# Optimization experiments

Measured on AMD Instinct MI355X. Metric: run time of the kernel, lower is better.

Reference implementation:

```python
import jax, jax.numpy as jnp
import numpy as np
import math

B, S, SIG, EMB, LAT, H, L_ENC, L_DEC = 16, 1024, 256, 256, 256, 8, 2, 2
EH, DH = EMB // H, LAT // H
EPS = 1e-10


def _sinusoidal_last_row(d):
    # last row of a standard sinusoidal PE table (position index = max_len-1)
    pos = 5000.0 - 1.0
    i = np.arange(d)
    angles = pos / np.power(10000.0, (2 * (i // 2)) / d)
    pe = np.where(i % 2 == 0, np.sin(angles), np.cos(angles))
    return jnp.asarray(pe, dtype=jnp.float32)


def setup_inputs() -> dict:
    key = jax.random.key(0)
    ks = iter(jax.random.split(key, 64))
    w = lambda *sh: 0.05 * jax.random.normal(next(ks), sh, dtype=jnp.float32)
    z = lambda *sh: jnp.zeros(sh, dtype=jnp.float32)
    d = {
        'inputData': jax.random.normal(next(ks), (B, S, SIG), dtype=jnp.float32),
        'pos_enc': _sinusoidal_last_row(SIG),
        'embW': w(SIG, EMB), 'embb': z(EMB),
        'qW': w(EMB, EMB), 'qb': z(EMB),
        'kW': w(EMB, EMB), 'kb': z(EMB),
        'vW': w(EMB, EMB), 'vb': z(EMB),
        'encBW': w(EH, EH), 'encBb': z(EH),
        'oW': w(EMB, EMB), 'ob': z(EMB),
        'ffe_W1': w(EMB, 2 * EMB), 'ffe_b1': z(2 * EMB),
        'ffe_W2': w(2 * EMB, EMB), 'ffe_b2': z(EMB),
        'lnSA_g': jnp.ones((L_ENC, EMB)), 'lnSA_b': z(L_ENC, EMB),
        'lnFF_g': jnp.ones((L_ENC, EMB)), 'lnFF_b': z(L_ENC, EMB),
        'start': w(1, LAT),
        'decQW': w(LAT, LAT), 'decQb': z(LAT),
        'decKW': w(EMB, EMB), 'decKb': z(EMB),
        'decVW': w(EMB, LAT), 'decVb': z(LAT),
        'decBW': w(EH + DH, DH), 'decBb': z(DH),
        'latW': w(LAT, LAT), 'latb': z(LAT),
        'ffd_W1': w(LAT, LAT // 2), 'ffd_b1': z(LAT // 2),
        'ffd_W2': w(LAT // 2, LAT), 'ffd_b2': z(LAT),
        'lnCA_g': jnp.ones((L_DEC, LAT)), 'lnCA_b': z(L_DEC, LAT),
        'lnLFF_g': jnp.ones((L_DEC, LAT)), 'lnLFF_b': z(L_DEC, LAT),
        'finW': w(LAT, LAT), 'finb': z(LAT),
    }
    return d


def _ln(x, g, b):
    m = x.mean(-1, keepdims=True)
    v = x.var(-1, keepdims=True)
    return (x - m) * jax.lax.rsqrt(v + EPS) * g + b


def _enc_attn(x, qW, qb, kW, kb, vW, vb, bW, bb, oW, ob):
    # x: (B,S,EMB) -> heads (B,H,S,EH)
    sp = lambda t: t.reshape(B, S, H, EH).transpose(0, 2, 1, 3)
    q, k, v = sp(x @ qW + qb), sp(x @ kW + kb), sp(x @ vW + vb)
    bk = k @ bW + bb                                   # bilinear key (B,H,S,EH)
    attn = jax.nn.softmax(jnp.einsum('bhqd,bhkd->bhqk', q, bk) / math.sqrt(EH), axis=-1)
    out = jnp.einsum('bhqk,bhkd->bhqd', attn, v)
    out = out.transpose(0, 2, 1, 3).reshape(B, S, EMB)
    return out @ oW + ob


def _dec_attn(enc, lat, qW, qb, kW, kb, vW, vb, bW, bb, oW, ob):
    # lat: (B,LAT) single query token; enc: (B,S,EMB)
    q = (lat @ qW + qb).reshape(B, 1, H, DH).transpose(0, 2, 1, 3)   # (B,H,1,DH)
    k = (enc @ kW + kb).reshape(B, S, H, EH).transpose(0, 2, 1, 3)   # (B,H,S,EH)
    v = (enc @ vW + vb).reshape(B, S, H, DH).transpose(0, 2, 1, 3)   # (B,H,S,DH)
    qcat = jnp.broadcast_to(q, (B, H, S, DH))
    kcat = jnp.concatenate([k, qcat], axis=-1)                       # (B,H,S,EH+DH)
    bk = kcat @ bW + bb                                              # (B,H,S,DH)
    attn = jax.nn.softmax(jnp.einsum('bhqd,bhkd->bhqk', q, bk) / math.sqrt(EH + DH), axis=-1)
    out = jnp.einsum('bhqk,bhkd->bhqd', attn, v)                     # (B,H,1,DH)
    out = out.transpose(0, 2, 1, 3).reshape(B, LAT)
    return out @ oW + ob


def reference(inputData, pos_enc, embW, embb, qW, qb, kW, kb, vW, vb, encBW, encBb,
              oW, ob, ffe_W1, ffe_b1, ffe_W2, ffe_b2, lnSA_g, lnSA_b, lnFF_g, lnFF_b,
              start, decQW, decQb, decKW, decKb, decVW, decVb, decBW, decBb,
              latW, latb, ffd_W1, ffd_b1, ffd_W2, ffd_b2, lnCA_g, lnCA_b,
              lnLFF_g, lnLFF_b, finW, finb):
    emb = (inputData + pos_enc) @ embW + embb          # (B,S,EMB)
    t = emb
    for l in range(L_ENC):
        n = _ln(t, lnSA_g[l], lnSA_b[l])
        a = _enc_attn(n, qW, qb, kW, kb, vW, vb, encBW, encBb, oW, ob) + n
        t = a + emb
        n2 = _ln(t, lnFF_g[l], lnFF_b[l])
        ff = jax.nn.selu(n2 @ ffe_W1 + ffe_b1) @ ffe_W2 + ffe_b2
        t = ff + n2
    init_lat = jnp.broadcast_to(start, (B, LAT))
    lat = init_lat
    for l in range(L_DEC):
        nl = _ln(init_lat, lnCA_g[l], lnCA_b[l])       # module always feeds initialLatentData
        lat = _dec_attn(t, nl, decQW, decQb, decKW, decKb, decVW, decVb,
                        decBW, decBb, latW, latb)
        nf = _ln(lat, lnLFF_g[l], lnLFF_b[l])
        lat = jax.nn.selu(nf @ ffd_W1 + ffd_b1) @ ffd_W2 + ffd_b2
    return lat @ finW + finb
```

## Files before the change

kernel.cpp:

```cpp
#include <hip/hip_runtime.h>
#include <hip/hip_bf16.h>
#include <math.h>

typedef __hip_bfloat16 bf16;

#define BB 16
#define SS 1024
#define NH 8
#define NR (BB*SS)
#define SZE ((size_t)NR*256)
#define RS 264
#define HS 520
#define KS2 136

typedef __attribute__((ext_vector_type(8))) short short8;
typedef __attribute__((ext_vector_type(4))) float f32x4;
typedef __attribute__((ext_vector_type(8))) unsigned short u16x8;
typedef __attribute__((ext_vector_type(4))) unsigned short u16x4;

__device__ __forceinline__ float bf2f(bf16 x){ return __bfloat162float(x); }
__device__ __forceinline__ bf16  f2bf(float x){ return __float2bfloat16(x); }
__device__ __forceinline__ unsigned short f2bfu(float x){
  bf16 t = __float2bfloat16(x); return *reinterpret_cast<unsigned short*>(&t);
}
__device__ __forceinline__ float bfu2f(unsigned short u){
  return __uint_as_float(((unsigned)u)<<16);
}

__device__ __forceinline__ float ldT(const float* p, size_t i){ return p[i]; }
__device__ __forceinline__ float ldT(const bf16*  p, size_t i){ return bf2f(p[i]); }
__device__ __forceinline__ void  stT(float* p, size_t i, float v){ p[i] = v; }
__device__ __forceinline__ void  stT(bf16*  p, size_t i, float v){ p[i] = f2bf(v); }

__device__ __forceinline__ float selu_f(float x){
  const float a = 1.6732632423543772f, sc = 1.0507009873554805f;
  return sc * (x > 0.f ? x : a * expm1f(x));
}

__device__ __forceinline__ void gload16(const void* g, void* l){
  __builtin_amdgcn_global_load_lds(
      (const __attribute__((address_space(1))) unsigned int*)g,
      (__attribute__((address_space(3))) unsigned int*)l, 16, 0, 0);
}

struct PtrPack { const void* p[43]; };
struct TabPack { int off[43]; int cnt[43]; int total; };
struct TrTab   { int srcOff[12]; int K[12]; int N[12]; int dstOff[12]; int total; };

__global__ __launch_bounds__(256) void k_canon(PtrPack ptrs, TabPack tab,
    float* __restrict__ dst, int* __restrict__ flagw)
{
  unsigned w0 = ((const unsigned*)ptrs.p[18])[0];
  int isbf = (w0 == 0x3F803F80u) ? 1 : 0;
  if (blockIdx.x == 0 && threadIdx.x == 0) *flagw = isbf;
  __shared__ int so[43], sn[43];
  int tid = threadIdx.x;
  if (tid < 43){ so[tid] = tab.off[tid]; sn[tid] = tab.cnt[tid]; }
  __syncthreads();
  int g = blockIdx.x*256 + tid;
  if (g >= tab.total) return;
  int seg = 1;
  while (seg < 42 && g >= so[seg] + sn[seg]) seg++;
  int li = g - so[seg];
  float v = isbf ? bf2f(((const bf16*)ptrs.p[seg])[li])
                 : ((const float*)ptrs.p[seg])[li];
  dst[g] = v;
}

__global__ __launch_bounds__(256) void k_transW(const float* __restrict__ wt,
    TrTab tt, unsigned short* __restrict__ dst)
{
  int g = blockIdx.x*256 + threadIdx.x;
  if (g >= tt.total) return;
  int seg = 0;
  while (seg < 11 && g >= tt.dstOff[seg] + tt.K[seg]*tt.N[seg]) seg++;
  int li = g - tt.dstOff[seg];
  int K = tt.K[seg], N = tt.N[seg];
  int n = li / K, k = li - n*K;
  dst[g] = f2bfu(wt[tt.srcOff[seg] + (size_t)k*N + n]);
}

template<int K, int LDA, int CT>
__device__ __forceinline__ void wave_gemmN(const unsigned short (*As)[LDA],
    const unsigned short* __restrict__ Wt, int n0, f32x4 acc[4][CT], int lane)
{
  int col = lane & 15, quad = lane >> 4;
  #pragma unroll
  for (int k0 = 0; k0 < K; k0 += 32){
    short8 a[4], b[CT];
    #pragma unroll
    for (int rt = 0; rt < 4; rt++)
      a[rt] = *(const short8*)(&As[rt*16 + col][k0 + quad*8]);
    #pragma unroll
    for (int ct = 0; ct < CT; ct++)
      b[ct] = *(const short8*)(&Wt[(size_t)(n0 + ct*16 + col)*K + k0 + quad*8]);
    #pragma unroll
    for (int rt = 0; rt < 4; rt++)
      #pragma unroll
      for (int ct = 0; ct < CT; ct++)
        acc[rt][ct] = __builtin_amdgcn_mfma_f32_16x16x32_bf16(a[rt], b[ct], acc[rt][ct], 0, 0, 0);
  }
}

template<int K, int LDA, int CT>
__device__ __forceinline__ void wave_gemmM32(const unsigned short (*As)[LDA],
    const unsigned short* __restrict__ Wt, int n0, f32x4 acc[2][CT], int lane)
{
  int col = lane & 15, quad = lane >> 4;
  #pragma unroll
  for (int k0 = 0; k0 < K; k0 += 32){
    short8 a[2], b[CT];
    #pragma unroll
    for (int rt = 0; rt < 2; rt++)
      a[rt] = *(const short8*)(&As[rt*16 + col][k0 + quad*8]);
    #pragma unroll
    for (int ct = 0; ct < CT; ct++)
      b[ct] = *(const short8*)(&Wt[(size_t)(n0 + ct*16 + col)*K + k0 + quad*8]);
    #pragma unroll
    for (int rt = 0; rt < 2; rt++)
      #pragma unroll
      for (int ct = 0; ct < CT; ct++)
        acc[rt][ct] = __builtin_amdgcn_mfma_f32_16x16x32_bf16(a[rt], b[ct], acc[rt][ct], 0, 0, 0);
  }
}

#define ZERO_ACC4(acc)  { _Pragma("unroll") for (int rt=0;rt<4;rt++){ _Pragma("unroll") for (int ct=0;ct<4;ct++) acc[rt][ct] = (f32x4){0.f,0.f,0.f,0.f}; } }
#define ZERO_ACC2(acc)  { _Pragma("unroll") for (int rt=0;rt<4;rt++){ _Pragma("unroll") for (int ct=0;ct<2;ct++) acc[rt][ct] = (f32x4){0.f,0.f,0.f,0.f}; } }
#define ZERO_ACC24(acc) { _Pragma("unroll") for (int rt=0;rt<2;rt++){ _Pragma("unroll") for (int ct=0;ct<4;ct++) acc[rt][ct] = (f32x4){0.f,0.f,0.f,0.f}; } }

#define EPI_BEGIN(e) { int rt = (e)>>4, ct = ((e)>>2)&3, r = (e)&3; \
    int lrow = rt*16 + quad*4 + r; int gcol0 = ct*16 + col; \
    float av = acc[rt][ct][r]; (void)lrow; (void)gcol0; (void)av;
#define EPI_END }

#define EPI32_BEGIN(e) { int rt = (e)>>4, ct = ((e)>>2)&3, r = (e)&3; \
    int lrow = rt*16 + quad*4 + r; int gcol0 = ct*16 + col; \
    float av = acc[rt][ct][r]; (void)lrow; (void)gcol0; (void)av;
#define EPI32_END }

template<int PRE, typename OT>
__global__ __launch_bounds__(256) void k_gemm_mfma(const void* __restrict__ A,
    const int* __restrict__ flagp, const float* __restrict__ pe,
    const unsigned short* __restrict__ Wt, const float* __restrict__ bias,
    OT* __restrict__ out)
{
  __shared__ __align__(16) unsigned short As[64][RS];
  int tid = threadIdx.x;
  int m = blockIdx.x & 255, nh = blockIdx.x >> 8;
  int row0 = m*64;
  if (PRE == 0){
    int f = *flagp;
    for (int jj = 0; jj < 64; jj++){
      int idx = tid + jj*256, row = idx>>8, c = idx&255;
      size_t g = (size_t)(row0+row)*256 + c;
      float x = f ? bf2f(((const bf16*)A)[g]) : ((const float*)A)[g];
      As[row][c] = f2bfu(x + pe[c]);
    }
  } else {
    for (int jj = 0; jj < 64; jj++){
      int idx = tid + jj*256, row = idx>>8, c = idx&255;
      As[row][c] = f2bfu(((const float*)A)[(size_t)(row0+row)*256 + c]);
    }
  }
  __syncthreads();
  int w = tid>>6, lane = tid&63, col = lane&15, quad = lane>>4;
  int n0 = nh*128 + w*32;
  f32x4 acc[4][2];
  ZERO_ACC2(acc);
  wave_gemmN<256, RS, 2>(As, Wt, n0, acc, lane);
  #pragma unroll
  for (int rt = 0; rt < 4; rt++){
    #pragma unroll
    for (int ct = 0; ct < 2; ct++){
      #pragma unroll
      for (int r = 0; r < 4; r++){
        int grow = row0 + rt*16 + quad*4 + r;
        int gcol = n0 + ct*16 + col;
        stT(out, (size_t)grow*256 + gcol, acc[rt][ct][r] + bias[gcol]);
      }
    }
  }
}

__global__ __launch_bounds__(256) void k_decKV(const float* __restrict__ A,
    const unsigned short* __restrict__ KWt, const float* __restrict__ kb,
    const unsigned short* __restrict__ VWt, const float* __restrict__ vb,
    bf16* __restrict__ ko, bf16* __restrict__ vo)
{
  __shared__ __align__(16) unsigned short As[64][RS];
  int tid = threadIdx.x;
  int m = blockIdx.x & 255, nh = blockIdx.x >> 8;
  int row0 = m*64;
  for (int jj = 0; jj < 64; jj++){
    int idx = tid + jj*256, row = idx>>8, c = idx&255;
    As[row][c] = f2bfu(A[(size_t)(row0+row)*256 + c]);
  }
  __syncthreads();
  int w = tid>>6, lane = tid&63, col = lane&15, quad = lane>>4;
  int n0 = nh*128 + w*32;
  f32x4 acc[4][2];
  ZERO_ACC2(acc);
  wave_gemmN<256, RS, 2>(As, KWt, n0, acc, lane);
  #pragma unroll
  for (int rt = 0; rt < 4; rt++){
    #pragma unroll
    for (int ct = 0; ct < 2; ct++){
      #pragma unroll
      for (int r = 0; r < 4; r++){
        int grow = row0 + rt*16 + quad*4 + r;
        int gcol = n0 + ct*16 + col;
        ko[(size_t)grow*256 + gcol] = f2bf(acc[rt][ct][r] + kb[gcol]);
      }
    }
  }
  ZERO_ACC2(acc);
  wave_gemmN<256, RS, 2>(As, VWt, n0, acc, lane);
  #pragma unroll
  for (int rt = 0; rt < 4; rt++){
    #pragma unroll
    for (int ct = 0; ct < 2; ct++){
      #pragma unroll
      for (int r = 0; r < 4; r++){
        int grow = row0 + rt*16 + quad*4 + r;
        int gcol = n0 + ct*16 + col;
        vo[(size_t)grow*256 + gcol] = f2bf(acc[rt][ct][r] + vb[gcol]);
      }
    }
  }
}

__global__ __launch_bounds__(256) void k_qkvbk_mfma(const float* __restrict__ tsrc,
    const float* __restrict__ lng, const float* __restrict__ lnb,
    const unsigned short* __restrict__ qWt, const float* __restrict__ qb,
    const unsigned short* __restrict__ kWt, const float* __restrict__ kb,
    const unsigned short* __restrict__ vWt, const float* __restrict__ vb,
    const unsigned short* __restrict__ encBWt, const float* __restrict__ Bb,
    bf16* __restrict__ qo, bf16* __restrict__ vo, bf16* __restrict__ bko)
{
  __shared__ __align__(16) unsigned short Ns[64][RS];
  __shared__ __align__(16) unsigned short Ks[64][KS2];
  __shared__ float mArr[64], rArr[64];
  int tid = threadIdx.x;
  int m = blockIdx.x & 255, nh = blockIdx.x >> 8;
  int row0 = m*64;
  int b = row0 >> 10, s0 = row0 & 1023;
  {
    int row = tid>>2, l4 = tid&3;
    const float* rp = tsrc + (size_t)(row0+row)*256;
    float s = 0.f, s2 = 0.f;
    for (int c = l4; c < 256; c += 4){ float x = rp[c]; s += x; s2 += x*x; }
    s  += __shfl_down(s, 2, 4);  s  += __shfl_down(s, 1, 4);
    s2 += __shfl_down(s2, 2, 4); s2 += __shfl_down(s2, 1, 4);
    if (l4 == 0){
      float mn = s*(1.f/256.f);
      float v = s2*(1.f/256.f) - mn*mn;
      mArr[row] = mn; rArr[row] = rsqrtf(fmaxf(v,0.f) + 1e-10f);
    }
  }
  __syncthreads();
  for (int jj = 0; jj < 64; jj++){
    int idx = tid + jj*256, row = idx>>8, c = idx&255;
    float x = tsrc[(size_t)(row0+row)*256 + c];
    Ns[row][c] = f2bfu((x - mArr[row])*rArr[row]*lng[c] + lnb[c]);
  }
  __syncthreads();
  int w = tid>>6, lane = tid&63, col = lane&15, quad = lane>>4;
  int n0 = nh*128 + w*32;
  f32x4 acc[4][2];
  ZERO_ACC2(acc);
  wave_gemmN<256, RS, 2>(Ns, qWt, n0, acc, lane);
  #pragma unroll
  for (int rt = 0; rt < 4; rt++){
    #pragma unroll
    for (int ct = 0; ct < 2; ct++){
      #pragma unroll
      for (int r = 0; r < 4; r++){
        int grow = row0 + rt*16 + quad*4 + r;
        int gcol = n0 + ct*16 + col;
        qo[(size_t)grow*256 + gcol] = f2bf(acc[rt][ct][r] + qb[gcol]);
      }
    }
  }
  ZERO_ACC2(acc);
  wave_gemmN<256, RS, 2>(Ns, vWt, n0, acc, lane);
  #pragma unroll
  for (int rt = 0; rt < 4; rt++){
    #pragma unroll
    for (int ct = 0; ct < 2; ct++){
      #pragma unroll
      for (int r = 0; r < 4; r++){
        int grow = row0 + rt*16 + quad*4 + r;
        int gcol = n0 + ct*16 + col;
        vo[(size_t)grow*256 + gcol] = f2bf(acc[rt][ct][r] + vb[gcol]);
      }
    }
  }
  ZERO_ACC2(acc);
  wave_gemmN<256, RS, 2>(Ns, kWt, n0, acc, lane);
  #pragma unroll
  for (int rt = 0; rt < 4; rt++){
    #pragma unroll
    for (int ct = 0; ct < 2; ct++){
      #pragma unroll
      for (int r = 0; r < 4; r++){
        int lrow = rt*16 + quad*4 + r;
        int lcol = w*32 + ct*16 + col;
        Ks[lrow][lcol] = f2bfu(acc[rt][ct][r] + kb[nh*128 + lcol]);
      }
    }
  }
  __syncthreads();
  int h = nh*4 + w;
  ZERO_ACC2(acc);
  #pragma unroll
  for (int ct = 0; ct < 2; ct++){
    short8 bfrag = *(const short8*)(&encBWt[(size_t)(ct*16 + col)*32 + quad*8]);
    #pragma unroll
    for (int rt = 0; rt < 4; rt++){
      short8 afrag = *(const short8*)(&Ks[rt*16 + col][w*32 + quad*8]);
      acc[rt][ct] = __builtin_amdgcn_mfma_f32_16x16x32_bf16(afrag, bfrag, acc[rt][ct], 0, 0, 0);
    }
  }
  #pragma unroll
  for (int rt = 0; rt < 4; rt++){
    #pragma unroll
    for (int ct = 0; ct < 2; ct++){
      #pragma unroll
      for (int r = 0; r < 4; r++){
        int srow = s0 + rt*16 + quad*4 + r;
        int d = ct*16 + col;
        bko[(((size_t)(b*NH+h))*SS + srow)*32 + d] = f2bf(acc[rt][ct][r] + Bb[d]);
      }
    }
  }
}

__global__ __launch_bounds__(256) void k_attn_mfma(
    const bf16* __restrict__ q, const bf16* __restrict__ bk,
    const bf16* __restrict__ v, bf16* __restrict__ ao)
{
  int bi = blockIdx.x;
  int qq = bi >> 7, b = (bi >> 3) & 15, h = bi & 7;
  int tid = threadIdx.x;
  int w = tid>>6, lane = tid&63;
  int quad = lane>>4, col = lane&15;
  int q0 = qq*256 + w*64;

  __shared__ __align__(16) unsigned short Ks2b[2][64][32];
  __shared__ __align__(16) unsigned short Vt2b[2][32][72];
  __shared__ __align__(16) unsigned short Ps[4][64][72];

  const float scale2 = 0.17677669529663687f * 1.4426950408889634f;
  short8 aq[4];
  #pragma unroll
  for (int rt = 0; rt < 4; rt++){
    const unsigned short* gq = (const unsigned short*)q
        + ((size_t)(b*SS + q0 + rt*16 + col))*256 + h*32 + quad*8;
    u16x8 qv = *(const u16x8*)gq;
    #pragma unroll
    for (int i=0;i<8;i++) aq[rt][i] = (short)f2bfu(bfu2f(qv[i])*scale2);
  }

  float l_r[4][4];
  f32x4 o0[4], o1[4];
  #pragma unroll
  for (int rt=0;rt<4;rt++){
    o0[rt] = (f32x4){0.f,0.f,0.f,0.f};
    o1[rt] = (f32x4){0.f,0.f,0.f,0.f};
    #pragma unroll
    for (int r=0;r<4;r++) l_r[rt][r] = 0.f;
  }

  u16x8 rK;
  u16x4 rV0, rV1;
  int vk0 = (tid>>3), vdg = (tid&7);
  int vk1 = ((tid+256)>>3), vdg1 = (tid&7);
  {
    const u16x8* srcK = (const u16x8*)((const unsigned short*)bk
        + (((size_t)(b*NH+h))*SS + 0)*32);
    rK = srcK[tid];
    rV0 = *(const u16x4*)((const unsigned short*)v
        + ((size_t)(b*SS + 0 + vk0))*256 + h*32 + vdg*4);
    rV1 = *(const u16x4*)((const unsigned short*)v
        + ((size_t)(b*SS + 0 + vk1))*256 + h*32 + vdg1*4);
  }

  for (int kt = 0; kt < 16; kt++){
    int cb = kt & 1;
    ((u16x8*)&Ks2b[cb][0][0])[tid] = rK;
    #pragma unroll
    for (int i=0;i<4;i++) Vt2b[cb][vdg*4+i][vk0] = rV0[i];
    #pragma unroll
    for (int i=0;i<4;i++) Vt2b[cb][vdg1*4+i][vk1] = rV1[i];
    __syncthreads();
    if (kt < 15){
      int nk = kt + 1;
      const u16x8* srcK = (const u16x8*)((const unsigned short*)bk
          + (((size_t)(b*NH+h))*SS + (size_t)nk*64)*32);
      rK = srcK[tid];
      rV0 = *(const u16x4*)((const unsigned short*)v
          + ((size_t)(b*SS + nk*64 + vk0))*256 + h*32 + vdg*4);
      rV1 = *(const u16x4*)((const unsigned short*)v
          + ((size_t)(b*SS + nk*64 + vk1))*256 + h*32 + vdg1*4);
    }
    short8 bk8[4];
    #pragma unroll
    for (int t4 = 0; t4 < 4; t4++)
      bk8[t4] = *(const short8*)(&Ks2b[cb][t4*16 + col][quad*8]);
    #pragma unroll
    for (int rt = 0; rt < 4; rt++){
      f32x4 s[4];
      #pragma unroll
      for (int t4 = 0; t4 < 4; t4++)
        s[t4] = __builtin_amdgcn_mfma_f32_16x16x32_bf16(aq[rt], bk8[t4],
                  (f32x4){0.f,0.f,0.f,0.f}, 0, 0, 0);
      #pragma unroll
      for (int r=0;r<4;r++){
        #pragma unroll
        for (int t4=0;t4<4;t4++){
          float pv = __builtin_amdgcn_exp2f(s[t4][r]);
          l_r[rt][r] += pv;
          Ps[w][rt*16 + quad*4 + r][t4*16 + col] =
              (unsigned short)(__float_as_uint(pv) >> 16);
        }
      }
    }
    short8 bv00 = *(const short8*)(&Vt2b[cb][col][quad*8]);
    short8 bv10 = *(const short8*)(&Vt2b[cb][col][32 + quad*8]);
    short8 bv01 = *(const short8*)(&Vt2b[cb][16+col][quad*8]);
    short8 bv11 = *(const short8*)(&Vt2b[cb][16+col][32 + quad*8]);
    #pragma unroll
    for (int rt = 0; rt < 4; rt++){
      short8 ap0 = *(const short8*)(&Ps[w][rt*16 + col][quad*8]);
      short8 ap1 = *(const short8*)(&Ps[w][rt*16 + col][32 + quad*8]);
      o0[rt] = __builtin_amdgcn_mfma_f32_16x16x32_bf16(ap0, bv00, o0[rt], 0, 0, 0);
      o0[rt] = __builtin_amdgcn_mfma_f32_16x16x32_bf16(ap1, bv10, o0[rt], 0, 0, 0);
      o1[rt] = __builtin_amdgcn_mfma_f32_16x16x32_bf16(ap0, bv01, o1[rt], 0, 0, 0);
      o1[rt] = __builtin_amdgcn_mfma_f32_16x16x32_bf16(ap1, bv11, o1[rt], 0, 0, 0);
    }
  }
  #pragma unroll
  for (int rt=0;rt<4;rt++){
    #pragma unroll
    for (int r=0;r<4;r++){
      float l = l_r[rt][r];
      #pragma unroll
      for (int msk=1; msk<16; msk<<=1) l += __shfl_xor(l, msk, 64);
      float inv = 1.f / l;
      int qrow = q0 + rt*16 + quad*4 + r;
      size_t o = ((size_t)(b*SS + qrow))*256 + h*32;
      ao[o + col]      = f2bf(o0[rt][r]*inv);
      ao[o + 16 + col] = f2bf(o1[rt][r]*inv);
    }
  }
}

__global__ __launch_bounds__(256) void k_oln_mfma(
    const float* __restrict__ tsrc, const float* __restrict__ emb,
    const bf16* __restrict__ ao,
    const float* __restrict__ lnSAg, const float* __restrict__ lnSAb,
    const unsigned short* __restrict__ oWt, const float* __restrict__ ob,
    const float* __restrict__ lnFFg, const float* __restrict__ lnFFb,
    bf16* __restrict__ n2o)
{
  __shared__ __align__(16) unsigned short Aos[32][RS];
  __shared__ __align__(16) unsigned short Tm[32][RS];
  __shared__ float mArr[32], rArr[32];
  int tid = threadIdx.x, row0 = blockIdx.x*32;
  {
    int row = tid>>3, l8 = tid&7;
    const float* rp = tsrc + (size_t)(row0+row)*256;
    float s = 0.f, s2 = 0.f;
    for (int c = l8; c < 256; c += 8){ float x = rp[c]; s += x; s2 += x*x; }
    s  += __shfl_down(s, 4, 8);  s  += __shfl_down(s, 2, 8);  s  += __shfl_down(s, 1, 8);
    s2 += __shfl_down(s2, 4, 8); s2 += __shfl_down(s2, 2, 8); s2 += __shfl_down(s2, 1, 8);
    if (l8 == 0){
      float m = s*(1.f/256.f);
      float v = s2*(1.f/256.f) - m*m;
      mArr[row] = m; rArr[row] = rsqrtf(fmaxf(v,0.f) + 1e-10f);
    }
  }
  for (int jj = 0; jj < 4; jj++){
    int idx = tid + jj*256;
    int row = idx>>5, c8 = idx&31;
    *(u16x8*)(&Aos[row][c8*8]) =
        *(const u16x8*)((const unsigned short*)ao + (size_t)(row0+row)*256 + c8*8);
  }
  __syncthreads();
  int w = tid>>6, lane = tid&63, col = lane&15, quad = lane>>4;
  f32x4 acc[2][4];
  ZERO_ACC24(acc);
  wave_gemmM32<256, RS, 4>(Aos, oWt, w*64, acc, lane);
  #pragma unroll
  for (int e = 0; e < 32; e++){
    EPI32_BEGIN(e)
    int gcol = w*64 + gcol0;
    size_t g = (size_t)(row0+lrow)*256 + gcol;
    float n1 = (tsrc[g] - mArr[lrow])*rArr[lrow]*lnSAg[gcol] + lnSAb[gcol];
    Tm[lrow][gcol] = f2bfu(av + ob[gcol] + n1 + emb[g]);
    EPI32_END
  }
  __syncthreads();
  {
    int row = tid>>3, l8 = tid&7;
    float s = 0.f, s2 = 0.f;
    for (int c = l8; c < 256; c += 8){ float x = bfu2f(Tm[row][c]); s += x; s2 += x*x; }
    s  += __shfl_down(s, 4, 8);  s  += __shfl_down(s, 2, 8);  s  += __shfl_down(s, 1, 8);
    s2 += __shfl_down(s2, 4, 8); s2 += __shfl_down(s2, 2, 8); s2 += __shfl_down(s2, 1, 8);
    if (l8 == 0){
      float m = s*(1.f/256.f);
      float v = s2*(1.f/256.f) - m*m;
      mArr[row] = m; rArr[row] = rsqrtf(fmaxf(v,0.f) + 1e-10f);
    }
  }
  __syncthreads();
  for (int jj = 0; jj < 32; jj++){
    int idx = tid + jj*256, row = idx>>8, c = idx&255;
    float x = bfu2f(Tm[row][c]);
    n2o[(size_t)(row0+row)*256 + c] =
        f2bf((x - mArr[row])*rArr[row]*lnFFg[c] + lnFFb[c]);
  }
}

#define FF_STAGE(B, KT) { \
  int k0 = (KT)*64; \
  _Pragma("unroll") \
  for (int i = 0; i < 4; i++){ int c = w*4 + i; \
    gload16(A  + (size_t)(row0 + c*8 + rsub)*KFULL + k0 + sgo, &As[B][c*512]); } \
  _Pragma("unroll") \
  for (int i = 0; i < 2; i++){ int c = w*2 + i; \
    gload16(Wb + (size_t)(n0   + c*8 + rsub)*KFULL + k0 + sgo, &Bs[B][c*512]); } }

#define FF_COMPUTE(B) { \
  _Pragma("unroll") \
  for (int kk = 0; kk < 2; kk++){ \
    short8 a[4], b2r[2]; \
    _Pragma("unroll") \
    for (int rt = 0; rt < 4; rt++) \
      a[rt] = *(const short8*)(&As[B][((wr*64 + rt*16 + col)<<6) + ((((kk<<2)|quad) ^ (col&7))<<3)]); \
    _Pragma("unroll") \
    for (int ct = 0; ct < 2; ct++) \
      b2r[ct] = *(const short8*)(&Bs[B][((wc*32 + ct*16 + col)<<6) + ((((kk<<2)|quad) ^ (col&7))<<3)]); \
    _Pragma("unroll") \
    for (int rt = 0; rt < 4; rt++) \
      _Pragma("unroll") \
      for (int ct = 0; ct < 2; ct++) \
        acc[rt][ct] = __builtin_amdgcn_mfma_f32_16x16x32_bf16(a[rt], b2r[ct], acc[rt][ct], 0, 0, 0); } }

template<int KFULL, int NFULL, int EPI>
__global__ __launch_bounds__(256) void k_ff_gemm(const bf16* __restrict__ A,
    const unsigned short* __restrict__ Wt, const float* __restrict__ bias,
    const bf16* __restrict__ res, void* __restrict__ outv)
{
  __shared__ __align__(16) unsigned short As[2][128*64];
  __shared__ __align__(16) unsigned short Bs[2][64*64];
  constexpr int NWG = 128 * (NFULL/64);
  constexpr int NKT = KFULL/64;
  int tid = threadIdx.x;
  int w = tid>>6, lane = tid&63;
  int col = lane&15, quad = lane>>4;
  int wr = w>>1, wc = w&1;
  int rsub = lane>>3;
  int sgo = (((lane&7) ^ rsub)<<3);
  int bid = blockIdx.x;
  int swz = (bid & 7)*(NWG>>3) + (bid >> 3);
  int mb = swz & 127, nb = swz >> 7;
  int row0 = mb*128, n0 = nb*64;
  const bf16* Wb = (const bf16*)Wt;

  f32x4 acc[4][2];
  ZERO_ACC2(acc);

  FF_STAGE(0, 0);
  __syncthreads();
  #pragma unroll
  for (int kt = 0; kt < NKT-1; kt++){
    int cb = kt & 1;
    FF_STAGE(cb^1, kt+1);
    FF_COMPUTE(cb);
    __syncthreads();
  }
  FF_COMPUTE((NKT-1)&1);

  if (EPI == 0){
    bf16* o = (bf16*)outv;
    #pragma unroll
    for (int rt = 0; rt < 4; rt++){
      #pragma unroll
      for (int ct = 0; ct < 2; ct++){
        #pragma unroll
        for (int r = 0; r < 4; r++){
          int grow = row0 + wr*64 + rt*16 + quad*4 + r;
          int gcol = n0 + wc*32 + ct*16 + col;
          o[(size_t)grow*NFULL + gcol] = f2bf(selu_f(acc[rt][ct][r] + bias[gcol]));
        }
      }
    }
  } else {
    float* o = (float*)outv;
    #pragma unroll
    for (int rt = 0; rt < 4; rt++){
      #pragma unroll
      for (int ct = 0; ct < 2; ct++){
        #pragma unroll
        for (int r = 0; r < 4; r++){
          int grow = row0 + wr*64 + rt*16 + quad*4 + r;
          int gcol = n0 + wc*32 + ct*16 + col;
          size_t g = (size_t)grow*NFULL + gcol;
          o[g] = acc[rt][ct][r] + bias[gcol] + bf2f(res[g]);
        }
      }
    }
  }
}

__global__ __launch_bounds__(256) void k_dec_head(const float* __restrict__ startp,
    const float* __restrict__ lng, const float* __restrict__ lnb,
    const float* __restrict__ decQW, const float* __restrict__ decQb,
    const float* __restrict__ decBW,
    float* __restrict__ s_q, float* __restrict__ s_qc)
{
  __shared__ float s1[256], s2[256], nl[256], qv[256];
  int t = threadIdx.x;
  float v = startp[t];
  s1[t]=v; s2[t]=v*v; __syncthreads();
  for (int s=128;s>0;s>>=1){
    if (t<s){ s1[t]+=s1[t+s]; s2[t]+=s2[t+s]; }
    __syncthreads();
  }
  float m = s1[0]*(1.f/256.f);
  float var = s2[0]*(1.f/256.f) - m*m;
  float r = rsqrtf(fmaxf(var,0.f) + 1e-10f);
  nl[t] = (v-m)*r*lng[t] + lnb[t];
  __syncthreads();
  float acc = decQb[t];
  for (int k=0;k<256;k++) acc += nl[k]*decQW[k*256+t];
  qv[t] = acc; s_q[t] = acc;
  __syncthreads();
  int h = t>>5, d = t&31;
  float a = 0.f;
  #pragma unroll 8
  for (int e=0;e<32;e++) a += qv[h*32+e]*decBW[(32+e)*32 + d];
  s_qc[t] = a;
}

__global__ __launch_bounds__(256) void k_bkdec_mfma(const bf16* __restrict__ kk,
    const float* __restrict__ qc, const unsigned short* __restrict__ decBWt,
    const float* __restrict__ Bb, bf16* __restrict__ bko)
{
  __shared__ __align__(16) unsigned short Ks[64][RS];
  int tid = threadIdx.x, row0 = blockIdx.x*64;
  int b = row0 >> 10, s0 = row0 & 1023;
  for (int jj = 0; jj < 8; jj++){
    int idx = tid + jj*256;
    int row = idx>>5, c8 = idx&31;
    *(u16x8*)(&Ks[row][c8*8]) =
        *(const u16x8*)((const unsigned short*)kk + (size_t)(row0+row)*256 + c8*8);
  }
  __syncthreads();
  int w = tid>>6, lane = tid&63, col = lane&15, quad = lane>>4;
  f32x4 acc[4][4];
  ZERO_ACC4(acc);
  #pragma unroll
  for (int ct = 0; ct < 4; ct++){
    int base = w*64 + ct*16;
    int h = base >> 5, d0 = base & 31;
    short8 bfrag = *(const short8*)(&decBWt[(size_t)(d0 + col)*32 + quad*8]);
    #pragma unroll
    for (int rt = 0; rt < 4; rt++){
      short8 afrag = *(const short8*)(&Ks[rt*16 + col][h*32 + quad*8]);
      acc[rt][ct] = __builtin_amdgcn_mfma_f32_16x16x32_bf16(afrag, bfrag, acc[rt][ct], 0, 0, 0);
    }
  }
  #pragma unroll
  for (int e = 0; e < 64; e++){
    EPI_BEGIN(e)
    int srow = s0 + lrow;
    int gcol = w*64 + gcol0;
    int h = gcol >> 5, d = gcol & 31;
    bko[(((size_t)(b*NH+h))*SS + srow)*32 + d] = f2bf(av + qc[gcol] + Bb[d]);
    EPI_END
  }
}

__global__ __launch_bounds__(256) void k_attn_dec(const float* __restrict__ q,
    const bf16* __restrict__ bk, const bf16* __restrict__ v,
    float* __restrict__ out)
{
  int h = blockIdx.x & 7, b = blockIdx.x >> 3;
  int tid = threadIdx.x;
  __shared__ float qs[32];
  __shared__ float sc[SS];
  __shared__ float red[256];
  if (tid < 32) qs[tid] = q[h*32 + tid] * (0.125f * 1.4426950408889634f);
  __syncthreads();
  float lsum = 0.f;
  for (int jj=0;jj<4;jj++){
    int j = tid*4 + jj;
    size_t base = (((size_t)(b*NH+h))*SS + j)*32;
    float s = 0.f;
    #pragma unroll
    for (int d=0;d<32;d++) s += qs[d]*bf2f(bk[base + d]);
    float e = __builtin_amdgcn_exp2f(s);
    sc[j] = e; lsum += e;
  }
  red[tid] = lsum; __syncthreads();
  for (int s=128;s>0;s>>=1){ if (tid<s) red[tid]+=red[tid+s]; __syncthreads(); }
  float gs = red[0];
  __syncthreads();
  int d = tid & 31, c = tid >> 5;
  float acc = 0.f;
  for (int j=c*128; j<c*128+128; j++)
    acc += sc[j]*bf2f(v[((size_t)(b*SS + j))*256 + h*32 + d]);
  red[c*32+d] = acc;
  __syncthreads();
  if (tid < 32){
    float s = 0.f;
    #pragma unroll
    for (int cc=0;cc<8;cc++) s += red[cc*32+tid];
    out[b*256 + h*32 + tid] = s / gs;
  }
}

__global__ __launch_bounds__(256) void k_dec_tail(const float* __restrict__ s_ao,
    const float* __restrict__ latW, const float* __restrict__ latb,
    const float* __restrict__ lng, const float* __restrict__ lnb,
    const float* __restrict__ W1, const float* __restrict__ b1,
    const float* __restrict__ W2, const float* __restrict__ b2,
    const float* __restrict__ finW, const float* __restrict__ finb,
    const int* __restrict__ flagp, void* __restrict__ outv)
{
  __shared__ float x[256], y[256], s1[256], s2[256];
  int t = threadIdx.x, b = blockIdx.x;
  x[t] = s_ao[b*256 + t];
  __syncthreads();
  float lat = latb[t];
  for (int k=0;k<256;k++) lat += x[k]*latW[k*256+t];
  s1[t]=lat; s2[t]=lat*lat; __syncthreads();
  for (int s=128;s>0;s>>=1){
    if (t<s){ s1[t]+=s1[t+s]; s2[t]+=s2[t+s]; }
    __syncthreads();
  }
  float m = s1[0]*(1.f/256.f);
  float var = s2[0]*(1.f/256.f) - m*m;
  float r = rsqrtf(fmaxf(var,0.f) + 1e-10f);
  y[t] = (lat-m)*r*lng[t] + lnb[t];
  __syncthreads();
  if (t < 128){
    float a2 = b1[t];
    for (int k=0;k<256;k++) a2 += y[k]*W1[k*128+t];
    x[t] = selu_f(a2);
  }
  __syncthreads();
  float a3 = b2[t];
  for (int k=0;k<128;k++) a3 += x[k]*W2[k*256+t];
  s1[t] = a3;
  __syncthreads();
  float o = finb[t];
  for (int k=0;k<256;k++) o += s1[k]*finW[k*256+t];
  size_t oi = (size_t)b*256 + t;
  if (*flagp) ((bf16*)outv)[oi] = f2bf(o);
  else        ((float*)outv)[oi] = o;
}

extern "C" void kernel_launch(void* const* d_in, const int* in_sizes, int n_in,
                              void* d_out, int out_size, void* d_ws, size_t ws_size,
                              hipStream_t stream)
{
  static const int cnts[43] = {
    0,256,65536,256,65536,256,65536,256,65536,256,1024,32,65536,256,
    131072,512,131072,256,512,512,512,512,256,65536,256,65536,256,65536,256,
    2048,32,65536,256,32768,128,32768,256,512,512,512,512,65536,256 };
  TabPack tab; int acc0 = 0;
  for (int i = 0; i < 43; i++){ tab.off[i] = acc0; tab.cnt[i] = cnts[i]; acc0 += cnts[i]; }
  tab.total = acc0;
  PtrPack ptrs;
  for (int i = 0; i < 43; i++) ptrs.p[i] = d_in[i];

  char* p = (char*)d_ws;
  float* wt   = (float*)p;
  int*  flagp = (int*)(p + (4u<<20));
  char* bigc  = p + (4u<<20) + 256;
  float* g_emb = (float*)bigc;
  float* g_t   = (float*)(bigc + SZE*4);
  bf16*  g_q   = (bf16*)(bigc + 2*SZE*4);
  bf16*  g_v   = (bf16*)(bigc + 2*SZE*4 + SZE*2);
  bf16*  g_ao  = (bf16*)(bigc + 2*SZE*4 + 2*SZE*2);
  bf16*  g_bk  = (bf16*)(bigc + 2*SZE*4 + 3*SZE*2);
  float* fsm   = (float*)(bigc + 2*SZE*4 + 4*SZE*2);
  unsigned short* wtr = (unsigned short*)(bigc + 2*SZE*4 + 4*SZE*2 + 131072*4);
  float* s_q  = fsm;
  float* s_qc = fsm + 256;
  float* s_ao = fsm + 512;
  bf16*  g_h1 = g_v;

  static const int trIdx[10] = {2,4,6,8,12,14,16,25,27,10};
  static const int trK[10]   = {256,256,256,256,256,256,512,256,256,32};
  static const int trN[10]   = {256,256,256,256,256,512,256,256,256,32};
  TrTab tr; int tacc = 0;
  for (int i = 0; i < 10; i++){
    tr.srcOff[i] = tab.off[trIdx[i]];
    tr.K[i] = trK[i]; tr.N[i] = trN[i];
    tr.dstOff[i] = tacc; tacc += trK[i]*trN[i];
  }
  tr.srcOff[10] = tab.off[29];        tr.K[10]=32; tr.N[10]=32; tr.dstOff[10]=tacc; tacc+=1024;
  tr.srcOff[11] = tab.off[29] + 1024; tr.K[11]=32; tr.N[11]=32; tr.dstOff[11]=tacc; tacc+=1024;
  tr.total = tacc;
  const unsigned short *embWt = wtr + tr.dstOff[0], *qWt = wtr + tr.dstOff[1],
    *kWt = wtr + tr.dstOff[2], *vWt = wtr + tr.dstOff[3], *oWt = wtr + tr.dstOff[4],
    *ffeW1t = wtr + tr.dstOff[5], *ffeW2t = wtr + tr.dstOff[6],
    *decKWt = wtr + tr.dstOff[7], *decVWt = wtr + tr.dstOff[8],
    *encBWt = wtr + tr.dstOff[9], *decBWtk = wtr + tr.dstOff[10];

  #define WP(i) (wt + tab.off[i])
  const float *pe=WP(1), *embb=WP(3), *qb=WP(5), *kb=WP(7), *vb=WP(9),
    *encBb=WP(11), *ob=WP(13), *ffeb1=WP(15), *ffeb2=WP(17),
    *lnSAg=WP(18), *lnSAb=WP(19), *lnFFg=WP(20), *lnFFb=WP(21),
    *startp=WP(22), *decQW=WP(23), *decQb=WP(24), *decKb=WP(26),
    *decVb=WP(28), *decBW=WP(29), *decBb=WP(30), *latW=WP(31),
    *latb=WP(32), *ffdW1=WP(33), *ffdb1=WP(34), *ffdW2=WP(35), *ffdb2=WP(36),
    *lnCAg=WP(37), *lnCAb=WP(38), *lnLFFg=WP(39), *lnLFFb=WP(40),
    *finW=WP(41), *finb=WP(42);

  dim3 blk(256);
  const int G64  = NR/64;
  const int G32  = NR/32;
  const int GSP  = 512;
  const int GA2  = 512;
  const int LD   = 1;

  k_canon<<<(tab.total+255)/256, blk, 0, stream>>>(ptrs, tab, wt, flagp);
  k_transW<<<(tr.total+255)/256, blk, 0, stream>>>(wt, tr, wtr);

  k_gemm_mfma<0,float><<<GSP, blk, 0, stream>>>(d_in[0], flagp, pe, embWt, embb, g_emb);

  const float* tcur = g_emb;
  for (int l = 0; l < 2; l++){
    k_qkvbk_mfma<<<GSP, blk, 0, stream>>>(tcur, lnSAg+l*256, lnSAb+l*256,
        qWt, qb, kWt, kb, vWt, vb, encBWt, encBb, g_q, g_v, g_bk);
    k_attn_mfma<<<GA2, blk, 0, stream>>>(g_q, g_bk, g_v, g_ao);
    k_oln_mfma<<<G32, blk, 0, stream>>>(tcur, g_emb, g_ao,
        lnSAg+l*256, lnSAb+l*256, oWt, ob, lnFFg+l*256, lnFFb+l*256, g_q);
    k_ff_gemm<256,512,0><<<1024, blk, 0, stream>>>(g_q, ffeW1t, ffeb1, (const bf16*)nullptr, g_h1);
    k_ff_gemm<512,256,1><<<512, blk, 0, stream>>>(g_h1, ffeW2t, ffeb2, g_q, g_t);
    tcur = g_t;
  }

  k_dec_head<<<1, blk, 0, stream>>>(startp, lnCAg+LD*256, lnCAb+LD*256,
      decQW, decQb, decBW, s_q, s_qc);
  k_decKV<<<GSP, blk, 0, stream>>>(g_t, decKWt, decKb, decVWt, decVb, g_q, g_v);
  k_bkdec_mfma<<<G64, blk, 0, stream>>>(g_q, s_qc, decBWtk, decBb, g_bk);
  k_attn_dec<<<BB*NH, blk, 0, stream>>>(s_q, g_bk, g_v, s_ao);
  k_dec_tail<<<BB, blk, 0, stream>>>(s_ao, latW, latb, lnLFFg+LD*256, lnLFFb+LD*256,
      ffdW1, ffdb1, ffdW2, ffdb2, finW, finb, flagp, d_out);
  #undef WP
}
```

Measured before the change: 514.0 us.

## Fold encoder key-projection matrix into Q weights and retile attention to 128-query blocks

The per-head key transform bW is precomputed into the query weights and bias with a new k_qfold kernel. This removes the LDS staging, extra barrier and small MFMA that computed k@bW inside the QKV kernel. The key bias term bb is dropped because it only adds a per-query constant, which softmax ignores. The attention kernel now uses 32 queries per wave with twice as many blocks, and gets XOR-swizzled K tiles in LDS and changed padding to cut bank conflicts. The trade-off is more K/V reloads per query across blocks and a small extra setup kernel.

```diff
diff --git a/kernel.cpp b/kernel.cpp
--- a/kernel.cpp
+++ b/kernel.cpp
@@ -11,7 +11,6 @@
 #define SZE ((size_t)NR*256)
 #define RS 264
 #define HS 520
-#define KS2 136
 
 typedef __attribute__((ext_vector_type(8))) short short8;
 typedef __attribute__((ext_vector_type(4))) float f32x4;
@@ -78,6 +77,27 @@
   int K = tt.K[seg], N = tt.N[seg];
   int n = li / K, k = li - n*K;
   dst[g] = f2bfu(wt[tt.srcOff[seg] + (size_t)k*N + n]);
+}
+
+__global__ __launch_bounds__(256) void k_qfold(const float* __restrict__ wt,
+    int qOff, int qbOff, int bwOff, unsigned short* __restrict__ qW2t,
+    float* __restrict__ qbf)
+{
+  __shared__ float bw[32];
+  int n = blockIdx.x, t = threadIdx.x;
+  int h = n>>5, d = n&31;
+  if (t < 32) bw[t] = wt[bwOff + d*32 + t];
+  __syncthreads();
+  float acc = 0.f;
+  #pragma unroll 8
+  for (int j = 0; j < 32; j++) acc += wt[qOff + (size_t)t*256 + h*32 + j]*bw[j];
+  qW2t[(size_t)n*256 + t] = f2bfu(acc);
+  if (t == 0){
+    float a = 0.f;
+    #pragma unroll 8
+    for (int j = 0; j < 32; j++) a += wt[qbOff + h*32 + j]*bw[j];
+    qbf[n] = a;
+  }
 }
 
 template<int K, int LDA, int CT>
@@ -231,14 +251,12 @@
 
 __global__ __launch_bounds__(256) void k_qkvbk_mfma(const float* __restrict__ tsrc,
     const float* __restrict__ lng, const float* __restrict__ lnb,
-    const unsigned short* __restrict__ qWt, const float* __restrict__ qb,
+    const unsigned short* __restrict__ qW2t, const float* __restrict__ qbf,
     const unsigned short* __restrict__ kWt, const float* __restrict__ kb,
     const unsigned short* __restrict__ vWt, const float* __restrict__ vb,
-    const unsigned short* __restrict__ encBWt, const float* __restrict__ Bb,
     bf16* __restrict__ qo, bf16* __restrict__ vo, bf16* __restrict__ bko)
 {
   __shared__ __align__(16) unsigned short Ns[64][RS];
-  __shared__ __align__(16) unsigned short Ks[64][KS2];
   __shared__ float mArr[64], rArr[64];
   int tid = threadIdx.x;
   int m = blockIdx.x & 255, nh = blockIdx.x >> 8;
@@ -268,7 +286,7 @@
   int n0 = nh*128 + w*32;
   f32x4 acc[4][2];
   ZERO_ACC2(acc);
-  wave_gemmN<256, RS, 2>(Ns, qWt, n0, acc, lane);
+  wave_gemmN<256, RS, 2>(Ns, qW2t, n0, acc, lane);
   #pragma unroll
   for (int rt = 0; rt < 4; rt++){
     #pragma unroll
@@ -277,7 +295,7 @@
       for (int r = 0; r < 4; r++){
         int grow = row0 + rt*16 + quad*4 + r;
         int gcol = n0 + ct*16 + col;
-        qo[(size_t)grow*256 + gcol] = f2bf(acc[rt][ct][r] + qb[gcol]);
+        qo[(size_t)grow*256 + gcol] = f2bf(acc[rt][ct][r] + qbf[gcol]);
       }
     }
   }
@@ -297,30 +315,7 @@
   }
   ZERO_ACC2(acc);
   wave_gemmN<256, RS, 2>(Ns, kWt, n0, acc, lane);
-  #pragma unroll
-  for (int rt = 0; rt < 4; rt++){
-    #pragma unroll
-    for (int ct = 0; ct < 2; ct++){
-      #pragma unroll
-      for (int r = 0; r < 4; r++){
-        int lrow = rt*16 + quad*4 + r;
-        int lcol = w*32 + ct*16 + col;
-        Ks[lrow][lcol] = f2bfu(acc[rt][ct][r] + kb[nh*128 + lcol]);
-      }
-    }
-  }
-  __syncthreads();
   int h = nh*4 + w;
-  ZERO_ACC2(acc);
-  #pragma unroll
-  for (int ct = 0; ct < 2; ct++){
-    short8 bfrag = *(const short8*)(&encBWt[(size_t)(ct*16 + col)*32 + quad*8]);
-    #pragma unroll
-    for (int rt = 0; rt < 4; rt++){
-      short8 afrag = *(const short8*)(&Ks[rt*16 + col][w*32 + quad*8]);
-      acc[rt][ct] = __builtin_amdgcn_mfma_f32_16x16x32_bf16(afrag, bfrag, acc[rt][ct], 0, 0, 0);
-    }
-  }
   #pragma unroll
   for (int rt = 0; rt < 4; rt++){
     #pragma unroll
@@ -329,7 +324,8 @@
       for (int r = 0; r < 4; r++){
         int srow = s0 + rt*16 + quad*4 + r;
         int d = ct*16 + col;
-        bko[(((size_t)(b*NH+h))*SS + srow)*32 + d] = f2bf(acc[rt][ct][r] + Bb[d]);
+        bko[(((size_t)(b*NH+h))*SS + srow)*32 + d] =
+            f2bf(acc[rt][ct][r] + kb[h*32 + d]);
       }
     }
   }
@@ -344,16 +340,16 @@
   int tid = threadIdx.x;
   int w = tid>>6, lane = tid&63;
   int quad = lane>>4, col = lane&15;
-  int q0 = qq*256 + w*64;
+  int q0 = qq*128 + w*32;
 
   __shared__ __align__(16) unsigned short Ks2b[2][64][32];
-  __shared__ __align__(16) unsigned short Vt2b[2][32][72];
-  __shared__ __align__(16) unsigned short Ps[4][64][72];
+  __shared__ __align__(16) unsigned short Vt2b[2][32][76];
+  __shared__ __align__(16) unsigned short Ps[4][32][68];
 
   const float scale2 = 0.17677669529663687f * 1.4426950408889634f;
-  short8 aq[4];
-  #pragma unroll
-  for (int rt = 0; rt < 4; rt++){
+  short8 aq[2];
+  #pragma unroll
+  for (int rt = 0; rt < 2; rt++){
     const unsigned short* gq = (const unsigned short*)q
         + ((size_t)(b*SS + q0 + rt*16 + col))*256 + h*32 + quad*8;
     u16x8 qv = *(const u16x8*)gq;
@@ -361,54 +357,53 @@
     for (int i=0;i<8;i++) aq[rt][i] = (short)f2bfu(bfu2f(qv[i])*scale2);
   }
 
-  float l_r[4][4];
-  f32x4 o0[4], o1[4];
-  #pragma unroll
-  for (int rt=0;rt<4;rt++){
+  float l_r[2][4];
+  f32x4 o0[2], o1[2];
+  #pragma unroll
+  for (int rt=0;rt<2;rt++){
     o0[rt] = (f32x4){0.f,0.f,0.f,0.f};
     o1[rt] = (f32x4){0.f,0.f,0.f,0.f};
     #pragma unroll
     for (int r=0;r<4;r++) l_r[rt][r] = 0.f;
   }
 
+  int krow = tid>>2, ksl = tid&3;
+  int kslw = ksl ^ ((krow>>1)&3);
+  int vk0 = tid>>3, vdg = tid&7;
+  int vk1 = vk0 + 32;
+  int rsl = (quad ^ ((col>>1)&3))*8;
+
+  const unsigned short* bkp = (const unsigned short*)bk + ((size_t)(b*NH+h))*SS*32;
+  const unsigned short* vp  = (const unsigned short*)v + (size_t)b*SS*256 + h*32;
+
   u16x8 rK;
   u16x4 rV0, rV1;
-  int vk0 = (tid>>3), vdg = (tid&7);
-  int vk1 = ((tid+256)>>3), vdg1 = (tid&7);
   {
-    const u16x8* srcK = (const u16x8*)((const unsigned short*)bk
-        + (((size_t)(b*NH+h))*SS + 0)*32);
-    rK = srcK[tid];
-    rV0 = *(const u16x4*)((const unsigned short*)v
-        + ((size_t)(b*SS + 0 + vk0))*256 + h*32 + vdg*4);
-    rV1 = *(const u16x4*)((const unsigned short*)v
-        + ((size_t)(b*SS + 0 + vk1))*256 + h*32 + vdg1*4);
+    rK  = *(const u16x8*)(bkp + (size_t)krow*32 + ksl*8);
+    rV0 = *(const u16x4*)(vp + (size_t)vk0*256 + vdg*4);
+    rV1 = *(const u16x4*)(vp + (size_t)vk1*256 + vdg*4);
   }
 
   for (int kt = 0; kt < 16; kt++){
     int cb = kt & 1;
-    ((u16x8*)&Ks2b[cb][0][0])[tid] = rK;
+    *(u16x8*)(&Ks2b[cb][krow][kslw*8]) = rK;
     #pragma unroll
     for (int i=0;i<4;i++) Vt2b[cb][vdg*4+i][vk0] = rV0[i];
     #pragma unroll
-    for (int i=0;i<4;i++) Vt2b[cb][vdg1*4+i][vk1] = rV1[i];
+    for (int i=0;i<4;i++) Vt2b[cb][vdg*4+i][vk1] = rV1[i];
     __syncthreads();
     if (kt < 15){
       int nk = kt + 1;
-      const u16x8* srcK = (const u16x8*)((const unsigned short*)bk
-          + (((size_t)(b*NH+h))*SS + (size_t)nk*64)*32);
-      rK = srcK[tid];
-      rV0 = *(const u16x4*)((const unsigned short*)v
-          + ((size_t)(b*SS + nk*64 + vk0))*256 + h*32 + vdg*4);
-      rV1 = *(const u16x4*)((const unsigned short*)v
-          + ((size_t)(b*SS + nk*64 + vk1))*256 + h*32 + vdg1*4);
+      rK  = *(const u16x8*)(bkp + (size_t)(nk*64 + krow)*32 + ksl*8);
+      rV0 = *(const u16x4*)(vp + (size_t)(nk*64 + vk0)*256 + vdg*4);
+      rV1 = *(const u16x4*)(vp + (size_t)(nk*64 + vk1)*256 + vdg*4);
     }
     short8 bk8[4];
     #pragma unroll
     for (int t4 = 0; t4 < 4; t4++)
-      bk8[t4] = *(const short8*)(&Ks2b[cb][t4*16 + col][quad*8]);
-    #pragma unroll
-    for (int rt = 0; rt < 4; rt++){
+      bk8[t4] = *(const short8*)(&Ks2b[cb][t4*16 + col][rsl]);
+    #pragma unroll
+    for (int rt = 0; rt < 2; rt++){
       f32x4 s[4];
       #pragma unroll
       for (int t4 = 0; t4 < 4; t4++)
@@ -430,7 +425,7 @@
     short8 bv01 = *(const short8*)(&Vt2b[cb][16+col][quad*8]);
     short8 bv11 = *(const short8*)(&Vt2b[cb][16+col][32 + quad*8]);
     #pragma unroll
-    for (int rt = 0; rt < 4; rt++){
+    for (int rt = 0; rt < 2; rt++){
       short8 ap0 = *(const short8*)(&Ps[w][rt*16 + col][quad*8]);
       short8 ap1 = *(const short8*)(&Ps[w][rt*16 + col][32 + quad*8]);
       o0[rt] = __builtin_amdgcn_mfma_f32_16x16x32_bf16(ap0, bv00, o0[rt], 0, 0, 0);
@@ -440,7 +435,7 @@
     }
   }
   #pragma unroll
-  for (int rt=0;rt<4;rt++){
+  for (int rt=0;rt<2;rt++){
     #pragma unroll
     for (int r=0;r<4;r++){
       float l = l_r[rt][r];
@@ -792,6 +787,7 @@
   float* s_q  = fsm;
   float* s_qc = fsm + 256;
   float* s_ao = fsm + 512;
+  float* qbf  = fsm + 8192;
   bf16*  g_h1 = g_v;
 
   static const int trIdx[10] = {2,4,6,8,12,14,16,25,27,10};
@@ -806,15 +802,16 @@
   tr.srcOff[10] = tab.off[29];        tr.K[10]=32; tr.N[10]=32; tr.dstOff[10]=tacc; tacc+=1024;
   tr.srcOff[11] = tab.off[29] + 1024; tr.K[11]=32; tr.N[11]=32; tr.dstOff[11]=tacc; tacc+=1024;
   tr.total = tacc;
-  const unsigned short *embWt = wtr + tr.dstOff[0], *qWt = wtr + tr.dstOff[1],
+  const unsigned short *embWt = wtr + tr.dstOff[0],
     *kWt = wtr + tr.dstOff[2], *vWt = wtr + tr.dstOff[3], *oWt = wtr + tr.dstOff[4],
     *ffeW1t = wtr + tr.dstOff[5], *ffeW2t = wtr + tr.dstOff[6],
     *decKWt = wtr + tr.dstOff[7], *decVWt = wtr + tr.dstOff[8],
-    *encBWt = wtr + tr.dstOff[9], *decBWtk = wtr + tr.dstOff[10];
+    *decBWtk = wtr + tr.dstOff[10];
+  unsigned short* qW2t = wtr + tr.total;
 
   #define WP(i) (wt + tab.off[i])
   const float *pe=WP(1), *embb=WP(3), *qb=WP(5), *kb=WP(7), *vb=WP(9),
-    *encBb=WP(11), *ob=WP(13), *ffeb1=WP(15), *ffeb2=WP(17),
+    *ob=WP(13), *ffeb1=WP(15), *ffeb2=WP(17),
     *lnSAg=WP(18), *lnSAb=WP(19), *lnFFg=WP(20), *lnFFb=WP(21),
     *startp=WP(22), *decQW=WP(23), *decQb=WP(24), *decKb=WP(26),
     *decVb=WP(28), *decBW=WP(29), *decBb=WP(30), *latW=WP(31),
@@ -826,18 +823,19 @@
   const int G64  = NR/64;
   const int G32  = NR/32;
   const int GSP  = 512;
-  const int GA2  = 512;
+  const int GA2  = 1024;
   const int LD   = 1;
 
   k_canon<<<(tab.total+255)/256, blk, 0, stream>>>(ptrs, tab, wt, flagp);
   k_transW<<<(tr.total+255)/256, blk, 0, stream>>>(wt, tr, wtr);
+  k_qfold<<<256, blk, 0, stream>>>(wt, tab.off[4], tab.off[5], tab.off[10], qW2t, qbf);
 
   k_gemm_mfma<0,float><<<GSP, blk, 0, stream>>>(d_in[0], flagp, pe, embWt, embb, g_emb);
 
   const float* tcur = g_emb;
   for (int l = 0; l < 2; l++){
     k_qkvbk_mfma<<<GSP, blk, 0, stream>>>(tcur, lnSAg+l*256, lnSAb+l*256,
-        qWt, qb, kWt, kb, vWt, vb, encBWt, encBb, g_q, g_v, g_bk);
+        qW2t, qbf, kWt, kb, vWt, vb, g_q, g_v, g_bk);
     k_attn_mfma<<<GA2, blk, 0, stream>>>(g_q, g_bk, g_v, g_ao);
     k_oln_mfma<<<G32, blk, 0, stream>>>(tcur, g_emb, g_ao,
         lnSAg+l*256, lnSAb+l*256, oWt, ob, lnFFg+l*256, lnFFb+l*256, g_q);
```

Result: no change. 522.8 us (+1.7%).
